# Performance work log

Hardware: AMD Instinct MI355X
Metric: run time of the kernel (lower is better)

The kernel has to match this reference:

```python
import jax, jax.numpy as jnp
import numpy as np

MEM = 128   # mem_dim
K = 4096    # number of object keys (each an array leaf list)
L = 128     # numbers per array
STATS_CAP = 100  # number_stats list capped at 100 entries


def setup_inputs() -> dict:
    key = jax.random.key(0)
    ks = jax.random.split(key, 13)
    s = 0.05
    return {
        "numbers": jax.random.normal(ks[0], (K, L), jnp.float32),
        "w_num": jax.random.normal(ks[1], (MEM,), jnp.float32) * s,
        "b_num": jax.random.normal(ks[2], (MEM,), jnp.float32) * s,
        "W_ih": jax.random.normal(ks[3], (4 * MEM, 2 * MEM), jnp.float32) * s,
        "W_hh": jax.random.normal(ks[4], (4 * MEM, MEM), jnp.float32) * s,
        "b_ih": jax.random.normal(ks[5], (4 * MEM,), jnp.float32) * s,
        "b_hh": jax.random.normal(ks[6], (4 * MEM,), jnp.float32) * s,
        "W_fh": jax.random.normal(ks[7], (MEM, MEM), jnp.float32) * s,
        "b_fh": jax.random.normal(ks[8], (MEM,), jnp.float32) * s,
        "W_iouh": jax.random.normal(ks[9], (3 * MEM, MEM), jnp.float32) * s,
        "b_iouh": jax.random.normal(ks[10], (3 * MEM,), jnp.float32) * s,
        "W_lout": jax.random.normal(ks[11], (MEM, MEM), jnp.float32) * s,
        "b_lout": jax.random.normal(ks[12], (MEM,), jnp.float32) * s,
    }


def _normalize_numbers(x_flat):
    # Replicates embed_number's running number_stats (tie_primitives -> one shared
    # '___default___' stats list, filled in traversal order, capped at 100 entries).
    # The k-th number is normalized by mean/std over the first min(k, 100) numbers
    # (including itself); std division only when len > 3 and std not ~0.
    n = x_flat.shape[0]
    k = jnp.arange(1, n + 1, dtype=jnp.float32)
    cs = jnp.cumsum(x_flat)
    css = jnp.cumsum(x_flat * x_flat)
    cap = jnp.minimum(k, float(STATS_CAP))
    cs_c = jnp.where(k <= STATS_CAP, cs, cs[STATS_CAP - 1])
    css_c = jnp.where(k <= STATS_CAP, css, css[STATS_CAP - 1])
    mean = cs_c / cap
    var = jnp.maximum(css_c / cap - mean * mean, 0.0)
    std = jnp.sqrt(var)
    # torch impl computes stats with numpy -> no gradient flows through them
    mean = jax.lax.stop_gradient(mean)
    std = jax.lax.stop_gradient(std)
    y = x_flat - mean
    use_std = (cap > 3.0) & (std > 1e-8)
    return jnp.where(use_std, y / jnp.where(use_std, std, 1.0), y)


def _forward(numbers, w_num, b_num, W_ih, W_hh, b_ih, b_hh,
             W_fh, b_fh, W_iouh, b_iouh, W_lout, b_lout):
    # --- embed_number: per-leaf (c=0, h = Linear(1, MEM)(norm_num)) ---
    x = _normalize_numbers(numbers.reshape(-1)).reshape(K, L)
    h_num = x[..., None] * w_num + b_num  # [K, L, MEM]

    # --- embed_array: LSTMCell over each array's children; input = cat([c_child, h_child]) ---
    # child_c is always 0 for number leaves.
    def step(carry, h_t):  # h_t: [K, MEM]
        c, h = carry
        xcat = jnp.concatenate([jnp.zeros_like(h_t), h_t], axis=-1)  # [K, 2*MEM]
        gates = xcat @ W_ih.T + b_ih + h @ W_hh.T + b_hh             # [K, 4*MEM]
        i, f, g, o = jnp.split(gates, 4, axis=-1)
        c2 = jax.nn.sigmoid(f) * c + jax.nn.sigmoid(i) * jnp.tanh(g)
        h2 = jax.nn.sigmoid(o) * jnp.tanh(c2)
        return (c2, h2), None

    z = jnp.zeros((K, MEM), numbers.dtype)
    (c_arr, h_arr), _ = jax.lax.scan(step, (z, z), jnp.swapaxes(h_num, 0, 1))
    # c_arr, h_arr: [K, MEM] final states per array child of the root object

    # --- embed_object (root): child-sum Tree-LSTM gating ---
    f_g = jax.nn.sigmoid(h_arr @ W_fh.T + b_fh)             # [K, MEM]
    fc_sum = jnp.sum(f_g * c_arr, axis=0, keepdims=True)    # [1, MEM]
    hs_bar = jnp.sum(h_arr, axis=0, keepdims=True)          # [1, MEM]
    iou = hs_bar @ W_iouh.T + b_iouh
    i, o, u = jnp.split(iou, 3, axis=-1)
    c = jax.nn.sigmoid(i) * jnp.tanh(u) + fc_sum
    h = jax.nn.sigmoid(o) * jnp.tanh(c)
    h_hat = h @ W_lout.T + b_lout
    return jnp.concatenate([c, h_hat], axis=1)  # [1, 2*MEM]


def reference(numbers, w_num, b_num, W_ih, W_hh, b_ih, b_hh,
              W_fh, b_fh, W_iouh, b_iouh, W_lout, b_lout):
    return _forward(numbers, w_num, b_num, W_ih, W_hh, b_ih, b_hh,
                    W_fh, b_fh, W_iouh, b_iouh, W_lout, b_lout)
```

## Files before the change

### kernel.cpp

```cpp
#include <hip/hip_runtime.h>
#include <math.h>

#define MEM 128
#define HSTR 136
#define LOG2E 1.4426950408889634f

typedef __bf16 bf16x8 __attribute__((ext_vector_type(8)));
typedef float  f32x4  __attribute__((ext_vector_type(4)));

__device__ __forceinline__ float fast_rcp(float x) { return __builtin_amdgcn_rcpf(x); }
__device__ __forceinline__ float fast_exp2(float x) { return __builtin_amdgcn_exp2f(x); }
__device__ __forceinline__ float fast_sigmoid(float x) {
    return fast_rcp(1.0f + fast_exp2(-LOG2E * x));
}
__device__ __forceinline__ float fast_tanh(float x) {
    return 2.0f * fast_rcp(1.0f + fast_exp2(-2.0f * LOG2E * x)) - 1.0f;
}

__global__ __launch_bounds__(512, 2) void fused_kernel(
        const float* __restrict__ numbers, const float* __restrict__ w_num,
        const float* __restrict__ b_num,   const float* __restrict__ W_ih,
        const float* __restrict__ W_hh,    const float* __restrict__ b_ih,
        const float* __restrict__ b_hh,    const float* __restrict__ W_fh,
        const float* __restrict__ b_fh,    const float* __restrict__ W_iouh,
        const float* __restrict__ b_iouh,  const float* __restrict__ W_lout,
        const float* __restrict__ b_lout,
        float* __restrict__ fc_sum, float* __restrict__ hs_bar,
        int* __restrict__ ticket, float* __restrict__ out) {
    __shared__ unsigned short hbuf[2][16 * HSTR];
    __shared__ float xls[128 * 16];
    __shared__ float mean_l[100], inv_l[100];
    __shared__ float abv[1024];
    __shared__ int   s_last;

    const int tid  = threadIdx.x;
    const int lane = tid & 63;
    const int wave = tid >> 6;
    const int quad = lane >> 4;
    const int lcol = lane & 15;
    const int m0   = wave * 16;
    const int r0   = blockIdx.x * 16;

    if (tid < 100) xls[tid] = numbers[tid];
    __syncthreads();
    if (tid < 100) {
        float s = 0.f, ss = 0.f;
        for (int j = 0; j <= tid; ++j) { float v = xls[j]; s += v; ss += v * v; }
        float cap  = (float)(tid + 1);
        float mean = s / cap;
        float var  = ss / cap - mean * mean;
        if (var < 0.f) var = 0.f;
        float sd = sqrtf(var);
        float inv = (cap > 3.0f && sd > 1e-8f) ? (1.0f / sd) : 1.0f;
        mean_l[tid] = mean;
        inv_l[tid]  = inv;
    }
    {
        const float* row = W_ih + tid * 256 + 128;
        float a = 0.f, b = 0.f;
        #pragma unroll
        for (int m = 0; m < 128; m += 4) {
            f32x4 w  = *(const f32x4*)(row + m);
            f32x4 wn = *(const f32x4*)(w_num + m);
            f32x4 bn = *(const f32x4*)(b_num + m);
            a += w[0] * wn[0] + w[1] * wn[1] + w[2] * wn[2] + w[3] * wn[3];
            b += w[0] * bn[0] + w[1] * bn[1] + w[2] * bn[2] + w[3] * bn[3];
        }
        abv[tid]       = a;
        abv[512 + tid] = b + b_ih[tid] + b_hh[tid];
    }
    __syncthreads();

    for (int i = tid; i < 16 * 128; i += 512) {
        int row = i >> 7;
        int t   = i & 127;
        int flat = (r0 + row) * 128 + t;
        int ii = (flat < 100) ? flat : 99;
        float v = numbers[flat];
        xls[t * 16 + row] = (v - mean_l[ii]) * inv_l[ii];
    }
    for (int i = tid; i < 16 * HSTR; i += 512) hbuf[0][i] = 0;

    const float GS[4] = { -LOG2E, -LOG2E, -2.0f * LOG2E, -LOG2E };

    bf16x8 bf[4][4];
    #pragma unroll
    for (int g = 0; g < 4; ++g) {
        #pragma unroll
        for (int kk = 0; kk < 4; ++kk) {
            int j = g * 128 + m0 + lcol;
            const float* p = W_hh + j * 128 + kk * 32 + quad * 8;
            f32x4 w0 = *(const f32x4*)p;
            f32x4 w1 = *(const f32x4*)(p + 4);
            bf16x8 bt;
            #pragma unroll
            for (int q = 0; q < 4; ++q) {
                bt[q]     = (__bf16)(w0[q] * GS[g]);
                bt[q + 4] = (__bf16)(w1[q] * GS[g]);
            }
            bf[g][kk] = bt;
        }
    }
    float ag[4], bg[4];
    #pragma unroll
    for (int g = 0; g < 4; ++g) {
        ag[g] = abv[g * 128 + m0 + lcol]       * GS[g];
        bg[g] = abv[512 + g * 128 + m0 + lcol] * GS[g];
    }

    float c[4]  = {0.f, 0.f, 0.f, 0.f};
    float hf[4] = {0.f, 0.f, 0.f, 0.f};
    __syncthreads();

    auto step = [&](int t, const unsigned short* hin, unsigned short* hout) {
        bf16x8 af[4];
        #pragma unroll
        for (int kk = 0; kk < 4; ++kk)
            af[kk] = *(const bf16x8*)(const void*)(hin + lcol * HSTR + kk * 32 + quad * 8);
        f32x4 xq = *(const f32x4*)(const void*)(xls + t * 16 + quad * 4);
        f32x4 acc[4];
        #pragma unroll
        for (int g = 0; g < 4; ++g) {
            f32x4 a0;
            #pragma unroll
            for (int r = 0; r < 4; ++r) a0[r] = xq[r] * ag[g] + bg[g];
            #pragma unroll
            for (int kk = 0; kk < 4; ++kk)
                a0 = __builtin_amdgcn_mfma_f32_16x16x32_bf16(af[kk], bf[g][kk], a0, 0, 0, 0);
            acc[g] = a0;
        }
        #pragma unroll
        for (int r = 0; r < 4; ++r) {
            float si = fast_rcp(1.0f + fast_exp2(acc[0][r]));
            float sf = fast_rcp(1.0f + fast_exp2(acc[1][r]));
            float rg = fast_rcp(1.0f + fast_exp2(acc[2][r]));
            float so = fast_rcp(1.0f + fast_exp2(acc[3][r]));
            float c2 = sf * c[r] + si * (2.0f * rg - 1.0f);
            c[r] = c2;
            float rc = fast_rcp(1.0f + fast_exp2(-2.0f * LOG2E * c2));
            float h  = so * (2.0f * rc - 1.0f);
            hf[r] = h;
            hout[(quad * 4 + r) * HSTR + m0 + lcol] = __builtin_bit_cast(unsigned short, (__bf16)h);
        }
        __syncthreads();
    };

    for (int t = 0; t < 128; t += 2) {
        step(t,     hbuf[0], hbuf[1]);
        step(t + 1, hbuf[1], hbuf[0]);
    }

    float v = hf[0] + hf[1] + hf[2] + hf[3];
    v += __shfl_xor(v, 16);
    v += __shfl_xor(v, 32);
    if (lane < 16) atomicAdd(&hs_bar[m0 + lane], v);

    f32x4 facc;
    {
        float bb = b_fh[m0 + lcol];
        #pragma unroll
        for (int r = 0; r < 4; ++r) facc[r] = bb;
    }
    #pragma unroll
    for (int kk = 0; kk < 4; ++kk) {
        bf16x8 afr = *(const bf16x8*)(const void*)(hbuf[0] + lcol * HSTR + kk * 32 + quad * 8);
        const float* p = W_fh + (m0 + lcol) * 128 + kk * 32 + quad * 8;
        f32x4 w0 = *(const f32x4*)p;
        f32x4 w1 = *(const f32x4*)(p + 4);
        bf16x8 wt;
        #pragma unroll
        for (int q = 0; q < 4; ++q) { wt[q] = (__bf16)w0[q]; wt[q + 4] = (__bf16)w1[q]; }
        facc = __builtin_amdgcn_mfma_f32_16x16x32_bf16(afr, wt, facc, 0, 0, 0);
    }
    float fcv = 0.f;
    #pragma unroll
    for (int r = 0; r < 4; ++r) fcv += fast_sigmoid(facc[r]) * c[r];
    fcv += __shfl_xor(fcv, 16);
    fcv += __shfl_xor(fcv, 32);
    if (lane < 16) atomicAdd(&fc_sum[m0 + lane], fcv);

    __threadfence();
    __syncthreads();
    if (tid == 0) {
        int old = atomicAdd(ticket, 1);
        s_last = (old == (int)gridDim.x - 1) ? 1 : 0;
    }
    __syncthreads();
    if (!s_last) return;

    __threadfence();
    float* hsb  = xls;
    float* iou  = xls + 128;
    float* hfin = xls + 512;
    if (tid < 128) hsb[tid] = atomicAdd(&hs_bar[tid], 0.0f);
    __syncthreads();
    const int part = tid & 3;
    const int jb   = tid >> 2;
    #pragma unroll
    for (int round = 0; round < 3; ++round) {
        int j = jb + round * 128;
        const float* row = W_iouh + j * 128 + part * 32;
        const float* hv  = hsb + part * 32;
        float s = 0.f;
        #pragma unroll
        for (int m = 0; m < 32; m += 4) {
            f32x4 w = *(const f32x4*)(row + m);
            s += w[0] * hv[m] + w[1] * hv[m + 1] + w[2] * hv[m + 2] + w[3] * hv[m + 3];
        }
        s += __shfl_xor(s, 1); s += __shfl_xor(s, 2);
        if (part == 0) iou[j] = s + b_iouh[j];
    }
    __syncthreads();
    if (tid < 128) {
        float fcr = atomicAdd(&fc_sum[tid], 0.0f);
        float i = iou[tid], o = iou[128 + tid], u = iou[256 + tid];
        float cf = fast_sigmoid(i) * fast_tanh(u) + fcr;
        out[tid] = cf;
        hfin[tid] = fast_sigmoid(o) * fast_tanh(cf);
    }
    __syncthreads();
    {
        const float* row = W_lout + jb * 128 + part * 32;
        const float* hv  = hfin + part * 32;
        float s = 0.f;
        #pragma unroll
        for (int m = 0; m < 32; m += 4) {
            f32x4 w = *(const f32x4*)(row + m);
            s += w[0] * hv[m] + w[1] * hv[m + 1] + w[2] * hv[m + 2] + w[3] * hv[m + 3];
        }
        s += __shfl_xor(s, 1); s += __shfl_xor(s, 2);
        if (part == 0) out[128 + jb] = s + b_lout[jb];
    }
}

extern "C" void kernel_launch(void* const* d_in, const int* in_sizes, int n_in,
                              void* d_out, int out_size, void* d_ws, size_t ws_size,
                              hipStream_t stream) {
    const float* numbers = (const float*)d_in[0];
    const float* w_num   = (const float*)d_in[1];
    const float* b_num   = (const float*)d_in[2];
    const float* W_ih    = (const float*)d_in[3];
    const float* W_hh    = (const float*)d_in[4];
    const float* b_ih    = (const float*)d_in[5];
    const float* b_hh    = (const float*)d_in[6];
    const float* W_fh    = (const float*)d_in[7];
    const float* b_fh    = (const float*)d_in[8];
    const float* W_iouh  = (const float*)d_in[9];
    const float* b_iouh  = (const float*)d_in[10];
    const float* W_lout  = (const float*)d_in[11];
    const float* b_lout  = (const float*)d_in[12];
    float* out = (float*)d_out;

    float* ws     = (float*)d_ws;
    float* fc_sum = ws;
    float* hs_bar = ws + 128;
    int*   ticket = (int*)(ws + 256);

    hipMemsetAsync(ws, 0, 257 * sizeof(float), stream);
    fused_kernel<<<256, 512, 0, stream>>>(numbers, w_num, b_num, W_ih, W_hh, b_ih, b_hh,
                                          W_fh, b_fh, W_iouh, b_iouh, W_lout, b_lout,
                                          fc_sum, hs_bar, ticket, out);
}
```

Before: 237.3 us.

## Split last-block ticket finalize into separate kernel and distribute input projection

Replaces the in-kernel ticket/last-block-done pattern with a second single-block finalize kernel, which removes the threadfence and global atomic ticket from every block. The W_ih·w_num projection is also recomputed per wave with a quad-split dot product and shuffle reduction, writing straight to registers. This drops the shared abv buffer and one __syncthreads. The cost is an extra kernel launch, and each block now reads its W_ih rows in a different pattern.

```diff
diff --git a/kernel.cpp b/kernel.cpp
--- a/kernel.cpp
+++ b/kernel.cpp
@@ -17,21 +17,16 @@
     return 2.0f * fast_rcp(1.0f + fast_exp2(-2.0f * LOG2E * x)) - 1.0f;
 }
 
-__global__ __launch_bounds__(512, 2) void fused_kernel(
+__global__ __launch_bounds__(512, 2) void lstm_kernel(
         const float* __restrict__ numbers, const float* __restrict__ w_num,
         const float* __restrict__ b_num,   const float* __restrict__ W_ih,
         const float* __restrict__ W_hh,    const float* __restrict__ b_ih,
         const float* __restrict__ b_hh,    const float* __restrict__ W_fh,
-        const float* __restrict__ b_fh,    const float* __restrict__ W_iouh,
-        const float* __restrict__ b_iouh,  const float* __restrict__ W_lout,
-        const float* __restrict__ b_lout,
-        float* __restrict__ fc_sum, float* __restrict__ hs_bar,
-        int* __restrict__ ticket, float* __restrict__ out) {
+        const float* __restrict__ b_fh,
+        float* __restrict__ fc_sum, float* __restrict__ hs_bar) {
     __shared__ unsigned short hbuf[2][16 * HSTR];
     __shared__ float xls[128 * 16];
     __shared__ float mean_l[100], inv_l[100];
-    __shared__ float abv[1024];
-    __shared__ int   s_last;
 
     const int tid  = threadIdx.x;
     const int lane = tid & 63;
@@ -55,21 +50,31 @@
         mean_l[tid] = mean;
         inv_l[tid]  = inv;
     }
-    {
-        const float* row = W_ih + tid * 256 + 128;
+    __syncthreads();
+
+    const float GS[4] = { -LOG2E, -LOG2E, -2.0f * LOG2E, -LOG2E };
+
+    float ag[4], bg[4];
+    #pragma unroll
+    for (int g = 0; g < 4; ++g) {
+        int j = g * 128 + m0 + lcol;
+        const float* row = W_ih + j * 256 + 128 + quad * 32;
+        const float* wn  = w_num + quad * 32;
+        const float* bn  = b_num + quad * 32;
         float a = 0.f, b = 0.f;
         #pragma unroll
-        for (int m = 0; m < 128; m += 4) {
+        for (int m = 0; m < 32; m += 4) {
             f32x4 w  = *(const f32x4*)(row + m);
-            f32x4 wn = *(const f32x4*)(w_num + m);
-            f32x4 bn = *(const f32x4*)(b_num + m);
-            a += w[0] * wn[0] + w[1] * wn[1] + w[2] * wn[2] + w[3] * wn[3];
-            b += w[0] * bn[0] + w[1] * bn[1] + w[2] * bn[2] + w[3] * bn[3];
-        }
-        abv[tid]       = a;
-        abv[512 + tid] = b + b_ih[tid] + b_hh[tid];
-    }
-    __syncthreads();
+            f32x4 vn = *(const f32x4*)(wn + m);
+            f32x4 vb = *(const f32x4*)(bn + m);
+            a += w[0] * vn[0] + w[1] * vn[1] + w[2] * vn[2] + w[3] * vn[3];
+            b += w[0] * vb[0] + w[1] * vb[1] + w[2] * vb[2] + w[3] * vb[3];
+        }
+        a += __shfl_xor(a, 16); a += __shfl_xor(a, 32);
+        b += __shfl_xor(b, 16); b += __shfl_xor(b, 32);
+        ag[g] = a * GS[g];
+        bg[g] = (b + b_ih[j] + b_hh[j]) * GS[g];
+    }
 
     for (int i = tid; i < 16 * 128; i += 512) {
         int row = i >> 7;
@@ -80,8 +85,6 @@
         xls[t * 16 + row] = (v - mean_l[ii]) * inv_l[ii];
     }
     for (int i = tid; i < 16 * HSTR; i += 512) hbuf[0][i] = 0;
-
-    const float GS[4] = { -LOG2E, -LOG2E, -2.0f * LOG2E, -LOG2E };
 
     bf16x8 bf[4][4];
     #pragma unroll
@@ -101,12 +104,6 @@
             bf[g][kk] = bt;
         }
     }
-    float ag[4], bg[4];
-    #pragma unroll
-    for (int g = 0; g < 4; ++g) {
-        ag[g] = abv[g * 128 + m0 + lcol]       * GS[g];
-        bg[g] = abv[512 + g * 128 + m0 + lcol] * GS[g];
-    }
 
     float c[4]  = {0.f, 0.f, 0.f, 0.f};
     float hf[4] = {0.f, 0.f, 0.f, 0.f};
@@ -178,24 +175,21 @@
     fcv += __shfl_xor(fcv, 16);
     fcv += __shfl_xor(fcv, 32);
     if (lane < 16) atomicAdd(&fc_sum[m0 + lane], fcv);
-
-    __threadfence();
-    __syncthreads();
-    if (tid == 0) {
-        int old = atomicAdd(ticket, 1);
-        s_last = (old == (int)gridDim.x - 1) ? 1 : 0;
-    }
-    __syncthreads();
-    if (!s_last) return;
-
-    __threadfence();
-    float* hsb  = xls;
-    float* iou  = xls + 128;
-    float* hfin = xls + 512;
-    if (tid < 128) hsb[tid] = atomicAdd(&hs_bar[tid], 0.0f);
-    __syncthreads();
+}
+
+__global__ void finalize_kernel(const float* __restrict__ fc_sum,
+                                const float* __restrict__ hs_bar,
+                                const float* __restrict__ W_iouh,
+                                const float* __restrict__ b_iouh,
+                                const float* __restrict__ W_lout,
+                                const float* __restrict__ b_lout,
+                                float* __restrict__ out) {
+    __shared__ float hsb[128], iou[384], hfin[128];
+    int tid = threadIdx.x;
     const int part = tid & 3;
     const int jb   = tid >> 2;
+    if (tid < 128) hsb[tid] = hs_bar[tid];
+    __syncthreads();
     #pragma unroll
     for (int round = 0; round < 3; ++round) {
         int j = jb + round * 128;
@@ -212,9 +206,8 @@
     }
     __syncthreads();
     if (tid < 128) {
-        float fcr = atomicAdd(&fc_sum[tid], 0.0f);
         float i = iou[tid], o = iou[128 + tid], u = iou[256 + tid];
-        float cf = fast_sigmoid(i) * fast_tanh(u) + fcr;
+        float cf = fast_sigmoid(i) * fast_tanh(u) + fc_sum[tid];
         out[tid] = cf;
         hfin[tid] = fast_sigmoid(o) * fast_tanh(cf);
     }
@@ -254,10 +247,10 @@
     float* ws     = (float*)d_ws;
     float* fc_sum = ws;
     float* hs_bar = ws + 128;
-    int*   ticket = (int*)(ws + 256);
-
-    hipMemsetAsync(ws, 0, 257 * sizeof(float), stream);
-    fused_kernel<<<256, 512, 0, stream>>>(numbers, w_num, b_num, W_ih, W_hh, b_ih, b_hh,
-                                          W_fh, b_fh, W_iouh, b_iouh, W_lout, b_lout,
-                                          fc_sum, hs_bar, ticket, out);
-}
+
+    hipMemsetAsync(ws, 0, 256 * sizeof(float), stream);
+    lstm_kernel<<<256, 512, 0, stream>>>(numbers, w_num, b_num, W_ih, W_hh, b_ih, b_hh,
+                                         W_fh, b_fh, fc_sum, hs_bar);
+    finalize_kernel<<<1, 512, 0, stream>>>(fc_sum, hs_bar, W_iouh, b_iouh,
+                                           W_lout, b_lout, out);
+}
```

Measured after the change: 214.2 us. 1.11x faster.
